# Kernel tuning notes

Hardware: AMD Instinct MI355X
Metric: run time of the kernel (lower is better)

The kernel has to match this reference:

```python
import jax, jax.numpy as jnp
import numpy as np

N_NODES = 1_000_000
D_IN = 128
GRAPH_STATE_DIM = 128  # node_hidden_sizes[-1] before doubling
N_GRAPHS = 4096


def setup_inputs() -> dict:
    key = jax.random.key(0)
    ks = jax.random.split(key, 10)
    s = lambda fan_in: 1.0 / np.sqrt(fan_in)
    return {
        "node_states": jax.random.normal(ks[0], (N_NODES, D_IN), dtype=jnp.float32),
        "graph_idx": jax.random.randint(ks[1], (N_NODES,), 0, N_GRAPHS),
        # MLP1: D_IN -> 64 -> 2*GRAPH_STATE_DIM
        "W1": jax.random.uniform(ks[2], (D_IN, 64), jnp.float32, -s(D_IN), s(D_IN)),
        "b1": jnp.zeros((64,), jnp.float32),
        "W2": jax.random.uniform(ks[3], (64, 2 * GRAPH_STATE_DIM), jnp.float32, -s(64), s(64)),
        "b2": jnp.zeros((2 * GRAPH_STATE_DIM,), jnp.float32),
        # MLP2: GRAPH_STATE_DIM -> 32 -> 16
        "W3": jax.random.uniform(ks[4], (GRAPH_STATE_DIM, 32), jnp.float32, -s(GRAPH_STATE_DIM), s(GRAPH_STATE_DIM)),
        "b3": jnp.zeros((32,), jnp.float32),
        "W4": jax.random.uniform(ks[5], (32, 16), jnp.float32, -s(32), s(32)),
        "b4": jnp.zeros((16,), jnp.float32),
    }


def reference(node_states, graph_idx, W1, b1, W2, b2, W3, b3, W4, b4):
    # MLP1: [N, D_IN] -> [N, 2*GRAPH_STATE_DIM]
    h = jax.nn.relu(node_states @ W1 + b1) @ W2 + b2
    gates = jax.nn.sigmoid(h[:, :GRAPH_STATE_DIM])
    gated = h[:, GRAPH_STATE_DIM:] * gates  # [N, GRAPH_STATE_DIM]
    # unsorted segment sum over graphs (n_graphs = max(graph_idx)+1 = N_GRAPHS)
    graph_states = jax.ops.segment_sum(gated, graph_idx, num_segments=N_GRAPHS)
    # MLP2: [G, GRAPH_STATE_DIM] -> [G, 16]
    out = jax.nn.relu(graph_states @ W3 + b3) @ W4 + b4
    return out
```

## Files before the change

kernel.cpp:

```cpp
#include <hip/hip_runtime.h>
#include <hip/hip_bf16.h>

#define N_NODES 1000000
#define D_IN 128
#define NG 4096
#define GSD 128
#define NGROUP_MAX 35232
#define K5_BLOCKS 8808

typedef __attribute__((ext_vector_type(4))) float f32x4;
typedef __attribute__((ext_vector_type(8))) short bf16x8;
typedef __attribute__((ext_vector_type(4))) int i32x4;

__device__ __forceinline__ short f2bs(float f) {
    unsigned u = __float_as_uint(f);
    u += 0x7FFF + ((u >> 16) & 1);
    return (short)(u >> 16);
}

__device__ __forceinline__ float sigmoid_fast(float x) {
    float e = __builtin_amdgcn_exp2f(-1.44269504089f * x);
    return __builtin_amdgcn_rcpf(1.0f + e);
}

__global__ void wconv_kernel(const float* __restrict__ W1, const float* __restrict__ W2,
                             short* __restrict__ w1t, short* __restrict__ w2t) {
    int idx = blockIdx.x * 256 + threadIdx.x;
    if (idx < 8192) {
        int n = idx >> 7, rem = idx & 127, c = rem >> 3, j = rem & 7;
        int k = ((c ^ (n & 15)) << 3) | j;
        w1t[idx] = f2bs(W1[k * 64 + n]);
    } else {
        int s = idx - 8192;
        int n = s >> 6, rem = s & 63, c = rem >> 3, j = rem & 7;
        int k = ((c ^ (n & 7)) << 3) | j;
        w2t[s] = f2bs(W2[k * 256 + n]);
    }
}

__global__ void hist_kernel(const int* __restrict__ gidx, int* __restrict__ cnt) {
    __shared__ int h[NG];
    int t = threadIdx.x;
    for (int i = t; i < NG; i += 256) h[i] = 0;
    __syncthreads();
    for (int i = blockIdx.x * 256 + t; i < N_NODES; i += gridDim.x * 256)
        atomicAdd(&h[gidx[i]], 1);
    __syncthreads();
    for (int i = t; i < NG; i += 256) {
        int v = h[i];
        if (v) atomicAdd(&cnt[i], v);
    }
}

__global__ __launch_bounds__(1024) void scan_kernel(const int* __restrict__ cnt,
                                                    int* __restrict__ poff,
                                                    int* __restrict__ ggid,
                                                    int* __restrict__ meta) {
    __shared__ int sc[1024];
    int t = threadIdx.x;
    int cc[4], c[4];
    int s = 0;
#pragma unroll
    for (int i = 0; i < 4; ++i) {
        cc[i] = cnt[t * 4 + i];
        c[i] = (cc[i] + 31) & ~31;
        s += c[i];
    }
    sc[t] = s;
    __syncthreads();
    for (int off = 1; off < 1024; off <<= 1) {
        int v = (t >= off) ? sc[t - off] : 0;
        __syncthreads();
        sc[t] += v;
        __syncthreads();
    }
    if (t == 1023) meta[0] = sc[1023] >> 5;
    int base = sc[t] - s;
#pragma unroll
    for (int i = 0; i < 4; ++i) {
        int g = t * 4 + i;
        poff[g] = base;
        int ngp = c[i] >> 5;
        int gb = base >> 5;
        for (int k = 0; k < ngp; ++k) {
            int rem = cc[i] - k * 32;
            int rows = rem > 32 ? 32 : rem;
            ggid[gb + k] = (g << 6) | (rows - 1);
        }
        base += c[i];
    }
}

__global__ void scatter_kernel(const int* __restrict__ gidx, const int* __restrict__ poff,
                               int* __restrict__ cur, int* __restrict__ order) {
    int i = blockIdx.x * 256 + threadIdx.x;
    if (i >= N_NODES) return;
    int g = gidx[i];
    int p = atomicAdd(&cur[g], 1);
    order[poff[g] + p] = i;
}

__global__ __launch_bounds__(256, 3) void main_kernel(
        const float* __restrict__ X, const short* __restrict__ w1t,
        const short* __restrict__ w2t, const float* __restrict__ b1,
        const float* __restrict__ b2, const int* __restrict__ order,
        const int* __restrict__ ggid, const int* __restrict__ meta,
        float* __restrict__ gs) {
    __shared__ __align__(16) short lds[24576];
    const int tid = threadIdx.x;

    for (int ci = tid; ci < 2048; ci += 256)
        *(i32x4*)&lds[ci * 8] = *(const i32x4*)&w2t[ci * 8];
    for (int ci = tid; ci < 1024; ci += 256)
        *(i32x4*)&lds[16384 + ci * 8] = *(const i32x4*)&w1t[ci * 8];

    const int wid = tid >> 6;
    const int w = (blockIdx.x << 2) + wid;
    const int lane = tid & 63;
    const int l15 = lane & 15;
    const int q = lane >> 4;
    const int ngroups = meta[0];
    const bool active = (w < ngroups);

    int g = 0, rows = 0;
    unsigned rowmask = 0;
    f32x4 acc1[2][4];

    __syncthreads();

    if (active) {
        int enc = ggid[w];
        g = enc >> 6;
        rows = (enc & 63) + 1;
        rowmask = (rows >= 32) ? 0xFFFFFFFFu : ((1u << rows) - 1u);
        bool v0 = l15 < rows;
        bool v1 = (16 + l15) < rows;
        int nd0r = order[w * 32 + l15];
        int nd1r = order[w * 32 + 16 + l15];
        const float* xp0 = X + (long long)(v0 ? nd0r : 0) * D_IN;
        const float* xp1 = X + (long long)(v1 ? nd1r : 0) * D_IN;

#pragma unroll
        for (int mt = 0; mt < 2; ++mt)
#pragma unroll
            for (int nt = 0; nt < 4; ++nt) acc1[mt][nt] = (f32x4){0.f, 0.f, 0.f, 0.f};

        const f32x4 z = {0.f, 0.f, 0.f, 0.f};
#pragma unroll
        for (int kk = 0; kk < 4; ++kk) {
            int koff = kk * 32 + q * 8;
            f32x4 x00 = v0 ? *(const f32x4*)(xp0 + koff) : z;
            f32x4 x01 = v0 ? *(const f32x4*)(xp0 + koff + 4) : z;
            f32x4 x10 = v1 ? *(const f32x4*)(xp1 + koff) : z;
            f32x4 x11 = v1 ? *(const f32x4*)(xp1 + koff + 4) : z;
            bf16x8 a0, a1;
#pragma unroll
            for (int j = 0; j < 4; ++j) {
                a0[j] = f2bs(x00[j]); a0[4 + j] = f2bs(x01[j]);
                a1[j] = f2bs(x10[j]); a1[4 + j] = f2bs(x11[j]);
            }
            int ch = (kk * 4 + q);
#pragma unroll
            for (int nt = 0; nt < 4; ++nt) {
                bf16x8 b = *(const bf16x8*)&lds[16384 + (nt * 16 + l15) * 128 + ((ch ^ l15) << 3)];
                acc1[0][nt] = __builtin_amdgcn_mfma_f32_16x16x32_bf16(a0, b, acc1[0][nt], 0, 0, 0);
                acc1[1][nt] = __builtin_amdgcn_mfma_f32_16x16x32_bf16(a1, b, acc1[1][nt], 0, 0, 0);
            }
        }
    }

    __syncthreads();

    const int h1b = 16384 + wid * 2048;
    if (active) {
#pragma unroll
        for (int nt = 0; nt < 4; ++nt) {
            float bb = b1[nt * 16 + l15];
            int c = nt * 2 + (l15 >> 3);
            int j7 = l15 & 7;
#pragma unroll
            for (int mt = 0; mt < 2; ++mt)
#pragma unroll
                for (int r = 0; r < 4; ++r) {
                    int m = mt * 16 + q * 4 + r;
                    float h = fmaxf(acc1[mt][nt][r] + bb, 0.f);
                    lds[h1b + m * 64 + ((c ^ (m & 7)) << 3) + j7] = f2bs(h);
                }
        }
    }

    __syncthreads();

    if (active) {
        bf16x8 A0[2], A1[2];
#pragma unroll
        for (int ks = 0; ks < 2; ++ks) {
            int ch = ((ks * 4 + q) ^ (l15 & 7)) << 3;
            A0[ks] = *(const bf16x8*)&lds[h1b + l15 * 64 + ch];
            A1[ks] = *(const bf16x8*)&lds[h1b + (16 + l15) * 64 + ch];
        }
#pragma unroll
        for (int nt = 0; nt < 8; ++nt) {
            f32x4 aG0 = (f32x4){0.f, 0.f, 0.f, 0.f}, aG1 = aG0, aV0 = aG0, aV1 = aG0;
#pragma unroll
            for (int ks = 0; ks < 2; ++ks) {
                int ch = ((ks * 4 + q) ^ (l15 & 7)) << 3;
                bf16x8 bG = *(const bf16x8*)&lds[(nt * 16 + l15) * 64 + ch];
                bf16x8 bV = *(const bf16x8*)&lds[((nt + 8) * 16 + l15) * 64 + ch];
                aG0 = __builtin_amdgcn_mfma_f32_16x16x32_bf16(A0[ks], bG, aG0, 0, 0, 0);
                aG1 = __builtin_amdgcn_mfma_f32_16x16x32_bf16(A1[ks], bG, aG1, 0, 0, 0);
                aV0 = __builtin_amdgcn_mfma_f32_16x16x32_bf16(A0[ks], bV, aV0, 0, 0, 0);
                aV1 = __builtin_amdgcn_mfma_f32_16x16x32_bf16(A1[ks], bV, aV1, 0, 0, 0);
            }
            float bg = b2[nt * 16 + l15];
            float bv = b2[128 + nt * 16 + l15];
            float s = 0.f;
#pragma unroll
            for (int mt = 0; mt < 2; ++mt) {
                f32x4 aG = mt ? aG1 : aG0;
                f32x4 aV = mt ? aV1 : aV0;
#pragma unroll
                for (int r = 0; r < 4; ++r) {
                    int row = mt * 16 + q * 4 + r;
                    float gate = sigmoid_fast(aG[r] + bg);
                    float gv = gate * (aV[r] + bv);
                    s += ((rowmask >> row) & 1u) ? gv : 0.f;
                }
            }
            s += __shfl_xor(s, 16);
            s += __shfl_xor(s, 32);
            if (lane < 16) unsafeAtomicAdd(&gs[(long long)g * GSD + nt * 16 + l15], s);
        }
    }
}

__global__ void mlp2_kernel(const float* __restrict__ gs, const float* __restrict__ W3,
                            const float* __restrict__ b3, const float* __restrict__ W4,
                            const float* __restrict__ b4, float* __restrict__ out) {
    __shared__ __align__(16) float sgs[8 * 128];
    __shared__ float sh3[8 * 32];
    int t = threadIdx.x;
    int g0 = blockIdx.x * 8;
    *(f32x4*)&sgs[t * 4] = *(const f32x4*)(gs + (long long)g0 * 128 + t * 4);
    __syncthreads();
    {
        int li = t >> 5, j = t & 31;
        float acc = b3[j];
#pragma unroll 8
        for (int k = 0; k < 128; ++k) acc += sgs[li * 128 + k] * W3[k * 32 + j];
        sh3[li * 32 + j] = fmaxf(acc, 0.f);
    }
    __syncthreads();
    if (t < 128) {
        int li = t >> 4, o = t & 15;
        float acc = b4[o];
#pragma unroll
        for (int j = 0; j < 32; ++j) acc += sh3[li * 32 + j] * W4[j * 16 + o];
        out[(g0 + li) * 16 + o] = acc;
    }
}

extern "C" void kernel_launch(void* const* d_in, const int* in_sizes, int n_in,
                              void* d_out, int out_size, void* d_ws, size_t ws_size,
                              hipStream_t stream) {
    (void)in_sizes; (void)n_in; (void)out_size; (void)ws_size;
    const float* X  = (const float*)d_in[0];
    const int* gidx = (const int*)d_in[1];
    const float* W1 = (const float*)d_in[2];
    const float* b1 = (const float*)d_in[3];
    const float* W2 = (const float*)d_in[4];
    const float* b2 = (const float*)d_in[5];
    const float* W3 = (const float*)d_in[6];
    const float* b3 = (const float*)d_in[7];
    const float* W4 = (const float*)d_in[8];
    const float* b4 = (const float*)d_in[9];
    float* out = (float*)d_out;

    char* ws   = (char*)d_ws;
    float* gs  = (float*)(ws + 0);
    int* cnt   = (int*)(ws + 2097152);
    int* cur   = (int*)(ws + 2113536);
    int* poff  = (int*)(ws + 2129920);
    int* meta  = (int*)(ws + 2146304);
    short* w1t = (short*)(ws + 2146368);
    short* w2t = (short*)(ws + 2162752);
    int* ggid  = (int*)(ws + 2195520);
    int* order = (int*)(ws + 2336448);

    hipMemsetAsync(ws, 0, 2129920, stream);

    wconv_kernel<<<96, 256, 0, stream>>>(W1, W2, w1t, w2t);
    hist_kernel<<<512, 256, 0, stream>>>(gidx, cnt);
    scan_kernel<<<1, 1024, 0, stream>>>(cnt, poff, ggid, meta);
    scatter_kernel<<<(N_NODES + 255) / 256, 256, 0, stream>>>(gidx, poff, cur, order);
    main_kernel<<<K5_BLOCKS, 256, 0, stream>>>(X, w1t, w2t, b1, b2, order, ggid, meta, gs);
    mlp2_kernel<<<512, 256, 0, stream>>>(gs, W3, b3, W4, b4, out);
}
```

Baseline: 858.3 us.

## Read weights from global instead of LDS, pad atomic counters, use packed bf16 convert

The main kernel no longer stages W1/W2 into shared memory. It reads weight fragments straight from global (cached) memory, which shrinks LDS to 16KB per block, drops a block-wide barrier, and raises the occupancy hint from 3 to 4. The count and cursor arrays are padded so each graph's atomic counter sits on its own 64-byte line, reducing contention between neighbouring counters. Float-to-bf16 conversion now uses the hardware packed instruction instead of manual rounding. Fetching weights from global on every MFMA step may cost more latency than the LDS reads it replaces, and the larger memset adds some traffic.

```diff
diff --git a/kernel.cpp b/kernel.cpp
--- a/kernel.cpp
+++ b/kernel.cpp
@@ -7,6 +7,7 @@
 #define GSD 128
 #define NGROUP_MAX 35232
 #define K5_BLOCKS 8808
+#define CPAD 16
 
 typedef __attribute__((ext_vector_type(4))) float f32x4;
 typedef __attribute__((ext_vector_type(8))) short bf16x8;
@@ -16,6 +17,12 @@
     unsigned u = __float_as_uint(f);
     u += 0x7FFF + ((u >> 16) & 1);
     return (short)(u >> 16);
+}
+
+__device__ __forceinline__ int cvt_pk_bf16(float lo, float hi) {
+    int r;
+    asm("v_cvt_pk_bf16_f32 %0, %1, %2" : "=v"(r) : "v"(lo), "v"(hi));
+    return r;
 }
 
 __device__ __forceinline__ float sigmoid_fast(float x) {
@@ -48,7 +55,7 @@
     __syncthreads();
     for (int i = t; i < NG; i += 256) {
         int v = h[i];
-        if (v) atomicAdd(&cnt[i], v);
+        if (v) atomicAdd(&cnt[i * CPAD], v);
     }
 }
 
@@ -62,7 +69,7 @@
     int s = 0;
 #pragma unroll
     for (int i = 0; i < 4; ++i) {
-        cc[i] = cnt[t * 4 + i];
+        cc[i] = cnt[(t * 4 + i) * CPAD];
         c[i] = (cc[i] + 31) & ~31;
         s += c[i];
     }
@@ -96,24 +103,18 @@
     int i = blockIdx.x * 256 + threadIdx.x;
     if (i >= N_NODES) return;
     int g = gidx[i];
-    int p = atomicAdd(&cur[g], 1);
+    int p = atomicAdd(&cur[g * CPAD], 1);
     order[poff[g] + p] = i;
 }
 
-__global__ __launch_bounds__(256, 3) void main_kernel(
+__global__ __launch_bounds__(256, 4) void main_kernel(
         const float* __restrict__ X, const short* __restrict__ w1t,
         const short* __restrict__ w2t, const float* __restrict__ b1,
         const float* __restrict__ b2, const int* __restrict__ order,
         const int* __restrict__ ggid, const int* __restrict__ meta,
         float* __restrict__ gs) {
-    __shared__ __align__(16) short lds[24576];
+    __shared__ __align__(16) short lds[8192];
     const int tid = threadIdx.x;
-
-    for (int ci = tid; ci < 2048; ci += 256)
-        *(i32x4*)&lds[ci * 8] = *(const i32x4*)&w2t[ci * 8];
-    for (int ci = tid; ci < 1024; ci += 256)
-        *(i32x4*)&lds[16384 + ci * 8] = *(const i32x4*)&w1t[ci * 8];
-
     const int wid = tid >> 6;
     const int w = (blockIdx.x << 2) + wid;
     const int lane = tid & 63;
@@ -121,17 +122,15 @@
     const int q = lane >> 4;
     const int ngroups = meta[0];
     const bool active = (w < ngroups);
-
-    int g = 0, rows = 0;
+    const int h1b = wid * 2048;
+
+    int g = 0;
     unsigned rowmask = 0;
-    f32x4 acc1[2][4];
-
-    __syncthreads();
 
     if (active) {
         int enc = ggid[w];
         g = enc >> 6;
-        rows = (enc & 63) + 1;
+        int rows = (enc & 63) + 1;
         rowmask = (rows >= 32) ? 0xFFFFFFFFu : ((1u << rows) - 1u);
         bool v0 = l15 < rows;
         bool v1 = (16 + l15) < rows;
@@ -140,6 +139,7 @@
         const float* xp0 = X + (long long)(v0 ? nd0r : 0) * D_IN;
         const float* xp1 = X + (long long)(v1 ? nd1r : 0) * D_IN;
 
+        f32x4 acc1[2][4];
 #pragma unroll
         for (int mt = 0; mt < 2; ++mt)
 #pragma unroll
@@ -153,26 +153,24 @@
             f32x4 x01 = v0 ? *(const f32x4*)(xp0 + koff + 4) : z;
             f32x4 x10 = v1 ? *(const f32x4*)(xp1 + koff) : z;
             f32x4 x11 = v1 ? *(const f32x4*)(xp1 + koff + 4) : z;
-            bf16x8 a0, a1;
-#pragma unroll
-            for (int j = 0; j < 4; ++j) {
-                a0[j] = f2bs(x00[j]); a0[4 + j] = f2bs(x01[j]);
-                a1[j] = f2bs(x10[j]); a1[4 + j] = f2bs(x11[j]);
+            union { bf16x8 v; int i[4]; } ua0, ua1;
+            ua0.i[0] = cvt_pk_bf16(x00[0], x00[1]);
+            ua0.i[1] = cvt_pk_bf16(x00[2], x00[3]);
+            ua0.i[2] = cvt_pk_bf16(x01[0], x01[1]);
+            ua0.i[3] = cvt_pk_bf16(x01[2], x01[3]);
+            ua1.i[0] = cvt_pk_bf16(x10[0], x10[1]);
+            ua1.i[1] = cvt_pk_bf16(x10[2], x10[3]);
+            ua1.i[2] = cvt_pk_bf16(x11[0], x11[1]);
+            ua1.i[3] = cvt_pk_bf16(x11[2], x11[3]);
+            int ch = kk * 4 + q;
+#pragma unroll
+            for (int nt = 0; nt < 4; ++nt) {
+                bf16x8 b = *(const bf16x8*)&w1t[(nt * 16 + l15) * 128 + ((ch ^ l15) << 3)];
+                acc1[0][nt] = __builtin_amdgcn_mfma_f32_16x16x32_bf16(ua0.v, b, acc1[0][nt], 0, 0, 0);
+                acc1[1][nt] = __builtin_amdgcn_mfma_f32_16x16x32_bf16(ua1.v, b, acc1[1][nt], 0, 0, 0);
             }
-            int ch = (kk * 4 + q);
-#pragma unroll
-            for (int nt = 0; nt < 4; ++nt) {
-                bf16x8 b = *(const bf16x8*)&lds[16384 + (nt * 16 + l15) * 128 + ((ch ^ l15) << 3)];
-                acc1[0][nt] = __builtin_amdgcn_mfma_f32_16x16x32_bf16(a0, b, acc1[0][nt], 0, 0, 0);
-                acc1[1][nt] = __builtin_amdgcn_mfma_f32_16x16x32_bf16(a1, b, acc1[1][nt], 0, 0, 0);
-            }
-        }
-    }
-
-    __syncthreads();
-
-    const int h1b = 16384 + wid * 2048;
-    if (active) {
+        }
+
 #pragma unroll
         for (int nt = 0; nt < 4; ++nt) {
             float bb = b1[nt * 16 + l15];
@@ -184,7 +182,7 @@
                 for (int r = 0; r < 4; ++r) {
                     int m = mt * 16 + q * 4 + r;
                     float h = fmaxf(acc1[mt][nt][r] + bb, 0.f);
-                    lds[h1b + m * 64 + ((c ^ (m & 7)) << 3) + j7] = f2bs(h);
+                    lds[h1b + m * 64 + ((c ^ (m & 7)) << 3) + j7] = (short)cvt_pk_bf16(h, h);
                 }
         }
     }
@@ -205,8 +203,8 @@
 #pragma unroll
             for (int ks = 0; ks < 2; ++ks) {
                 int ch = ((ks * 4 + q) ^ (l15 & 7)) << 3;
-                bf16x8 bG = *(const bf16x8*)&lds[(nt * 16 + l15) * 64 + ch];
-                bf16x8 bV = *(const bf16x8*)&lds[((nt + 8) * 16 + l15) * 64 + ch];
+                bf16x8 bG = *(const bf16x8*)&w2t[(nt * 16 + l15) * 64 + ch];
+                bf16x8 bV = *(const bf16x8*)&w2t[((nt + 8) * 16 + l15) * 64 + ch];
                 aG0 = __builtin_amdgcn_mfma_f32_16x16x32_bf16(A0[ks], bG, aG0, 0, 0, 0);
                 aG1 = __builtin_amdgcn_mfma_f32_16x16x32_bf16(A1[ks], bG, aG1, 0, 0, 0);
                 aV0 = __builtin_amdgcn_mfma_f32_16x16x32_bf16(A0[ks], bV, aV0, 0, 0, 0);
@@ -279,15 +277,15 @@
     char* ws   = (char*)d_ws;
     float* gs  = (float*)(ws + 0);
     int* cnt   = (int*)(ws + 2097152);
-    int* cur   = (int*)(ws + 2113536);
-    int* poff  = (int*)(ws + 2129920);
-    int* meta  = (int*)(ws + 2146304);
-    short* w1t = (short*)(ws + 2146368);
-    short* w2t = (short*)(ws + 2162752);
-    int* ggid  = (int*)(ws + 2195520);
-    int* order = (int*)(ws + 2336448);
-
-    hipMemsetAsync(ws, 0, 2129920, stream);
+    int* cur   = (int*)(ws + 2359296);
+    int* poff  = (int*)(ws + 2621440);
+    int* meta  = (int*)(ws + 2637824);
+    short* w1t = (short*)(ws + 2637888);
+    short* w2t = (short*)(ws + 2654272);
+    int* ggid  = (int*)(ws + 2687040);
+    int* order = (int*)(ws + 2827968);
+
+    hipMemsetAsync(ws, 0, 2621440, stream);
 
     wconv_kernel<<<96, 256, 0, stream>>>(W1, W2, w1t, w2t);
     hist_kernel<<<512, 256, 0, stream>>>(gidx, cnt);
```

After: 839.1 us. 1.02x faster.
